# Performance work log

Hardware: AMD Instinct MI355X
Metric: run time of the kernel (lower is better)

## Reference

```python
import jax, jax.numpy as jnp
import numpy as np

No_, Nk_, Ni_, D_, F_ = 256, 32, 512, 3, 64

def _quat_scale_to_covar(quats, scales):
    # gsplat convention: quat = (w, x, y, z), normalized; covar = R diag(s^2) R^T
    q = quats / jnp.linalg.norm(quats, axis=-1, keepdims=True)
    w, x, y, z = q[..., 0], q[..., 1], q[..., 2], q[..., 3]
    R = jnp.stack([
        1 - 2 * (y * y + z * z), 2 * (x * y - w * z), 2 * (x * z + w * y),
        2 * (x * y + w * z), 1 - 2 * (x * x + z * z), 2 * (y * z - w * x),
        2 * (x * z - w * y), 2 * (y * z + w * x), 1 - 2 * (x * x + y * y),
    ], axis=-1).reshape(q.shape[:-1] + (3, 3))
    M = R * scales[..., None, :]
    return M @ jnp.swapaxes(M, -1, -2)

def setup_inputs():
    key = jax.random.key(0)
    ks = jax.random.split(key, 8)
    weights = jax.random.uniform(ks[0], (Ni_,)) + 0.1          # positive mixture weights
    means = jax.random.normal(ks[1], (Ni_, D_))
    A = jax.random.normal(ks[2], (Ni_, D_, D_)) * 0.3
    covars = A @ jnp.swapaxes(A, -1, -2) + 0.1 * jnp.eye(D_)   # SPD input covariances
    features = jax.random.normal(ks[3], (Ni_, F_))
    k_weights = jax.random.uniform(ks[4], (No_, Nk_)) + 0.1
    k_means = jax.random.normal(ks[5], (No_, Nk_, D_))
    k_scales = jax.random.uniform(ks[6], (No_, Nk_, D_)) * 0.5 + 0.1
    k_quats = jax.random.normal(ks[7], (No_, Nk_, 4))
    return dict(weights=weights, means=means, covars=covars, features=features,
                k_weights=k_weights, k_means=k_means, k_scales=k_scales, k_quats=k_quats)

def reference(weights, means, covars, features, k_weights, k_means, k_scales, k_quats):
    No, Nk, D = k_means.shape
    # _sample: deterministic 'most important points' = means of top-No weighted components
    _, idx = jax.lax.top_k(weights, No)
    anchor = means[idx]                                   # (No, D)
    comp_means = anchor[:, None, :] + k_means             # (No, Nk, D)
    comp_covars = _quat_scale_to_covar(k_quats, k_scales) # (No, Nk, D, D)
    # GM convolution: outer-product broadcast over input components
    conv_w = k_weights[:, :, None] * weights[None, None, :]               # (No, Nk, Ni)
    conv_m = comp_means[:, :, None, :] + means[None, None, :, :]          # (No, Nk, Ni, D)
    conv_c = comp_covars[:, :, None, :, :] + covars[None, None, :, :, :]  # (No, Nk, Ni, D, D)
    # Moment-matching merge over the Ni axis (dim=2)
    W = conv_w.sum(-1)                                                    # (No, Nk)
    mu = jnp.einsum('oki,okid->okd', conv_w, conv_m) / W[..., None]       # (No, Nk, D)
    diff = conv_m - mu[:, :, None, :]
    second = conv_c + diff[..., :, None] * diff[..., None, :]
    cov = jnp.einsum('oki,okide->okde', conv_w, second) / W[..., None, None]  # (No, Nk, D, D)
    return W, mu, cov
```

## Files before the change

### kernel.cpp

```cpp
#include <hip/hip_runtime.h>

namespace {

constexpr int NO  = 256;
constexpr int NK  = 32;
constexpr int NI  = 512;
constexpr int BLK = 1024;
constexpr int NB  = (NO * NK) / BLK;

using u32 = unsigned int;
using u64 = unsigned long long;

__global__ __launch_bounds__(BLK) void gm_fused_kernel(
    const float* __restrict__ weights,
    const float* __restrict__ means,
    const float* __restrict__ covars,
    const float* __restrict__ k_weights,
    const float* __restrict__ k_means,
    const float* __restrict__ k_scales,
    const float* __restrict__ k_quats,
    float* __restrict__ out)
{
  __shared__ __align__(16) u64 keys[NI];
  __shared__ int   rhi[NI];
  __shared__ float anchors[NO * 3];
  __shared__ float red[16][6];
  __shared__ float stats[10];

  const int tid   = threadIdx.x;
  const int lane  = tid & 63;
  const int wave  = tid >> 6;
  const bool lower = tid < NI;
  const int item  = lower ? tid : tid - NI;

  const int t = blockIdx.x * BLK + tid;
  const int o = t >> 5;
  const float  kw  = k_weights[t];
  const float  km0 = k_means[3 * t + 0];
  const float  km1 = k_means[3 * t + 1];
  const float  km2 = k_means[3 * t + 2];
  const float4 q4  = *(const float4*)(k_quats + 4 * t);
  const float  s0  = k_scales[3 * t + 0];
  const float  s1  = k_scales[3 * t + 1];
  const float  s2  = k_scales[3 * t + 2];

  const float w  = weights[item];
  const float m0 = means[3 * item + 0];
  const float m1 = means[3 * item + 1];
  const float m2 = means[3 * item + 2];

  float acc[6] = {0.f, 0.f, 0.f, 0.f, 0.f, 0.f};
  if (lower) {
    acc[0] = w;
    acc[1] = w * m0; acc[2] = w * m1; acc[3] = w * m2;
    keys[item] = ((u64)__float_as_uint(w) << 32) | (u32)(NI - 1 - item);
  } else {
    const float c00 = covars[9 * item + 0];
    const float c01 = covars[9 * item + 1];
    const float c02 = covars[9 * item + 2];
    const float c11 = covars[9 * item + 4];
    const float c12 = covars[9 * item + 5];
    const float c22 = covars[9 * item + 8];
    acc[0] = w * (c00 + m0 * m0);
    acc[1] = w * (c01 + m0 * m1);
    acc[2] = w * (c02 + m0 * m2);
    acc[3] = w * (c11 + m1 * m1);
    acc[4] = w * (c12 + m1 * m2);
    acc[5] = w * (c22 + m2 * m2);
  }

  #pragma unroll
  for (int off = 32; off > 0; off >>= 1) {
    #pragma unroll
    for (int e = 0; e < 6; ++e) acc[e] += __shfl_down(acc[e], off, 64);
  }
  if (lane == 0) {
    #pragma unroll
    for (int e = 0; e < 6; ++e) red[wave][e] = acc[e];
  }
  __syncthreads();

  if (tid < 10) {
    float s = 0.f;
    if (tid < 4) {
      #pragma unroll
      for (int wv = 0; wv < 8; ++wv) s += red[wv][tid];
    } else {
      #pragma unroll
      for (int wv = 8; wv < 16; ++wv) s += red[wv][tid - 4];
    }
    stats[tid] = s;
  }

  const u64 mykey = keys[item];
  const ulonglong2* seg = (const ulonglong2*)(keys + (lower ? 0 : NI / 2));
  int r = 0;
  #pragma unroll 8
  for (int p = 0; p < (NI / 2) / 2; ++p) {
    const ulonglong2 kk = seg[p];
    r += (int)(kk.x > mykey);
    r += (int)(kk.y > mykey);
  }
  if (!lower) rhi[item] = r;
  __syncthreads();

  if (lower) {
    const int rank = r + rhi[item];
    if (rank < NO) {
      anchors[3 * rank + 0] = m0;
      anchors[3 * rank + 1] = m1;
      anchors[3 * rank + 2] = m2;
    }
  }
  __syncthreads();

  const float S   = stats[0];
  const float inv = 1.f / S;
  const float b0 = stats[1] * inv, b1 = stats[2] * inv, b2 = stats[3] * inv;
  const float C00 = stats[4] * inv - b0 * b0;
  const float C01 = stats[5] * inv - b0 * b1;
  const float C02 = stats[6] * inv - b0 * b2;
  const float C11 = stats[7] * inv - b1 * b1;
  const float C12 = stats[8] * inv - b1 * b2;
  const float C22 = stats[9] * inv - b2 * b2;
  const float a0 = anchors[3 * o + 0];
  const float a1 = anchors[3 * o + 1];
  const float a2 = anchors[3 * o + 2];

  float qw = q4.x, qx = q4.y, qy = q4.z, qz = q4.w;
  const float rn = rsqrtf(qw * qw + qx * qx + qy * qy + qz * qz);
  qw *= rn; qx *= rn; qy *= rn; qz *= rn;

  float R[3][3];
  R[0][0] = 1.f - 2.f * (qy * qy + qz * qz);
  R[0][1] = 2.f * (qx * qy - qw * qz);
  R[0][2] = 2.f * (qx * qz + qw * qy);
  R[1][0] = 2.f * (qx * qy + qw * qz);
  R[1][1] = 1.f - 2.f * (qx * qx + qz * qz);
  R[1][2] = 2.f * (qy * qz - qw * qx);
  R[2][0] = 2.f * (qx * qz - qw * qy);
  R[2][1] = 2.f * (qy * qz + qw * qx);
  R[2][2] = 1.f - 2.f * (qx * qx + qy * qy);

  const float sc[3] = { s0, s1, s2 };
  float M[3][3];
  #pragma unroll
  for (int rr = 0; rr < 3; ++rr)
    #pragma unroll
    for (int cc = 0; cc < 3; ++cc)
      M[rr][cc] = R[rr][cc] * sc[cc];

  const float Cb[9] = { C00, C01, C02, C01, C11, C12, C02, C12, C22 };
  float cov[9];
  #pragma unroll
  for (int rr = 0; rr < 3; ++rr) {
    #pragma unroll
    for (int cc = 0; cc < 3; ++cc) {
      float a = Cb[3 * rr + cc];
      #pragma unroll
      for (int e = 0; e < 3; ++e) a += M[rr][e] * M[cc][e];
      cov[3 * rr + cc] = a;
    }
  }

  out[t] = kw * S;
  const int mu_base = NO * NK + 3 * t;
  out[mu_base + 0] = a0 + km0 + b0;
  out[mu_base + 1] = a1 + km1 + b1;
  out[mu_base + 2] = a2 + km2 + b2;
  const int cov_base = NO * NK * 4 + 9 * t;
  #pragma unroll
  for (int e = 0; e < 9; ++e)
    out[cov_base + e] = cov[e];
}

}

extern "C" void kernel_launch(void* const* d_in, const int* in_sizes, int n_in,
                              void* d_out, int out_size, void* d_ws, size_t ws_size,
                              hipStream_t stream) {
  const float* weights   = (const float*)d_in[0];
  const float* means     = (const float*)d_in[1];
  const float* covars    = (const float*)d_in[2];
  const float* k_weights = (const float*)d_in[4];
  const float* k_means   = (const float*)d_in[5];
  const float* k_scales  = (const float*)d_in[6];
  const float* k_quats   = (const float*)d_in[7];

  gm_fused_kernel<<<NB, BLK, 0, stream>>>(weights, means, covars,
                                          k_weights, k_means, k_scales, k_quats,
                                          (float*)d_out);
}
```

Before: 14.23 us.

## Halve block size, rank all keys per thread, keep only block-local anchors

Moves from 8 blocks of 1024 threads to 16 blocks of 512 threads. Each thread now loads two input components and computes the full rank of its key against all 512 keys, instead of splitting the count across two half-threads and combining them through shared memory. Each block stores only the 16 anchors its outputs need, which drops one barrier and the rank-combining array. The cost is a per-thread ranking loop twice as long, plus every block repeating the top-k and statistics work.

```diff
diff --git a/kernel.cpp b/kernel.cpp
--- a/kernel.cpp
+++ b/kernel.cpp
@@ -2,11 +2,12 @@
 
 namespace {
 
-constexpr int NO  = 256;
-constexpr int NK  = 32;
-constexpr int NI  = 512;
-constexpr int BLK = 1024;
-constexpr int NB  = (NO * NK) / BLK;
+constexpr int NO   = 256;
+constexpr int NK   = 32;
+constexpr int NI   = 512;
+constexpr int BLK  = 512;
+constexpr int NB   = (NO * NK) / BLK;
+constexpr int OWIN = BLK / NK;
 
 using u32 = unsigned int;
 using u64 = unsigned long long;
@@ -22,19 +23,17 @@
     float* __restrict__ out)
 {
   __shared__ __align__(16) u64 keys[NI];
-  __shared__ int   rhi[NI];
-  __shared__ float anchors[NO * 3];
-  __shared__ float red[16][6];
+  __shared__ float sm[NI * 3];
+  __shared__ float anchors[OWIN * 3];
+  __shared__ float red[8][6];
   __shared__ float stats[10];
 
-  const int tid   = threadIdx.x;
-  const int lane  = tid & 63;
-  const int wave  = tid >> 6;
-  const bool lower = tid < NI;
-  const int item  = lower ? tid : tid - NI;
+  const int tid  = threadIdx.x;
+  const int lane = tid & 63;
+  const int wave = tid >> 6;
+  const int b    = blockIdx.x;
 
-  const int t = blockIdx.x * BLK + tid;
-  const int o = t >> 5;
+  const int t = b * BLK + tid;
   const float  kw  = k_weights[t];
   const float  km0 = k_means[3 * t + 0];
   const float  km1 = k_means[3 * t + 1];
@@ -44,29 +43,36 @@
   const float  s1  = k_scales[3 * t + 1];
   const float  s2  = k_scales[3 * t + 2];
 
-  const float w  = weights[item];
-  const float m0 = means[3 * item + 0];
-  const float m1 = means[3 * item + 1];
-  const float m2 = means[3 * item + 2];
+  const bool lowgrp = tid < 256;
+  const int  ia     = lowgrp ? tid : tid - 256;
 
   float acc[6] = {0.f, 0.f, 0.f, 0.f, 0.f, 0.f};
-  if (lower) {
-    acc[0] = w;
-    acc[1] = w * m0; acc[2] = w * m1; acc[3] = w * m2;
-    keys[item] = ((u64)__float_as_uint(w) << 32) | (u32)(NI - 1 - item);
-  } else {
-    const float c00 = covars[9 * item + 0];
-    const float c01 = covars[9 * item + 1];
-    const float c02 = covars[9 * item + 2];
-    const float c11 = covars[9 * item + 4];
-    const float c12 = covars[9 * item + 5];
-    const float c22 = covars[9 * item + 8];
-    acc[0] = w * (c00 + m0 * m0);
-    acc[1] = w * (c01 + m0 * m1);
-    acc[2] = w * (c02 + m0 * m2);
-    acc[3] = w * (c11 + m1 * m1);
-    acc[4] = w * (c12 + m1 * m2);
-    acc[5] = w * (c22 + m2 * m2);
+  #pragma unroll
+  for (int rr = 0; rr < 2; ++rr) {
+    const int i = ia + 256 * rr;
+    const float w  = weights[i];
+    const float m0 = means[3 * i + 0];
+    const float m1 = means[3 * i + 1];
+    const float m2 = means[3 * i + 2];
+    if (lowgrp) {
+      acc[0] += w;
+      acc[1] += w * m0; acc[2] += w * m1; acc[3] += w * m2;
+      keys[i] = ((u64)__float_as_uint(w) << 32) | (u32)(NI - 1 - i);
+      sm[3 * i + 0] = m0; sm[3 * i + 1] = m1; sm[3 * i + 2] = m2;
+    } else {
+      const float c00 = covars[9 * i + 0];
+      const float c01 = covars[9 * i + 1];
+      const float c02 = covars[9 * i + 2];
+      const float c11 = covars[9 * i + 4];
+      const float c12 = covars[9 * i + 5];
+      const float c22 = covars[9 * i + 8];
+      acc[0] += w * (c00 + m0 * m0);
+      acc[1] += w * (c01 + m0 * m1);
+      acc[2] += w * (c02 + m0 * m2);
+      acc[3] += w * (c11 + m1 * m1);
+      acc[4] += w * (c12 + m1 * m2);
+      acc[5] += w * (c22 + m2 * m2);
+    }
   }
 
   #pragma unroll
@@ -84,33 +90,28 @@
     float s = 0.f;
     if (tid < 4) {
       #pragma unroll
-      for (int wv = 0; wv < 8; ++wv) s += red[wv][tid];
+      for (int wv = 0; wv < 4; ++wv) s += red[wv][tid];
     } else {
       #pragma unroll
-      for (int wv = 8; wv < 16; ++wv) s += red[wv][tid - 4];
+      for (int wv = 4; wv < 8; ++wv) s += red[wv][tid - 4];
     }
     stats[tid] = s;
   }
 
-  const u64 mykey = keys[item];
-  const ulonglong2* seg = (const ulonglong2*)(keys + (lower ? 0 : NI / 2));
+  const u64 mykey = keys[tid];
+  const ulonglong2* seg = (const ulonglong2*)keys;
   int r = 0;
-  #pragma unroll 8
-  for (int p = 0; p < (NI / 2) / 2; ++p) {
+  #pragma unroll 16
+  for (int p = 0; p < NI / 2; ++p) {
     const ulonglong2 kk = seg[p];
     r += (int)(kk.x > mykey);
     r += (int)(kk.y > mykey);
   }
-  if (!lower) rhi[item] = r;
-  __syncthreads();
-
-  if (lower) {
-    const int rank = r + rhi[item];
-    if (rank < NO) {
-      anchors[3 * rank + 0] = m0;
-      anchors[3 * rank + 1] = m1;
-      anchors[3 * rank + 2] = m2;
-    }
+  const int lr = r - OWIN * b;
+  if ((unsigned)lr < (unsigned)OWIN) {
+    anchors[3 * lr + 0] = sm[3 * tid + 0];
+    anchors[3 * lr + 1] = sm[3 * tid + 1];
+    anchors[3 * lr + 2] = sm[3 * tid + 2];
   }
   __syncthreads();
 
@@ -123,9 +124,11 @@
   const float C11 = stats[7] * inv - b1 * b1;
   const float C12 = stats[8] * inv - b1 * b2;
   const float C22 = stats[9] * inv - b2 * b2;
-  const float a0 = anchors[3 * o + 0];
-  const float a1 = anchors[3 * o + 1];
-  const float a2 = anchors[3 * o + 2];
+
+  const int ol = tid >> 5;
+  const float a0 = anchors[3 * ol + 0];
+  const float a1 = anchors[3 * ol + 1];
+  const float a2 = anchors[3 * ol + 2];
 
   float qw = q4.x, qx = q4.y, qy = q4.z, qz = q4.w;
   const float rn = rsqrtf(qw * qw + qx * qx + qy * qy + qz * qz);
```

Measured after the change: 18.35 us. 28.9% more time.
